# Performance work log

Measured on AMD Instinct MI355X. Metric: run time of the kernel, lower is better.

Reference implementation:

```python
import jax, jax.numpy as jnp
import numpy as np

HIDDEN = 1024
D_COMPLEX = HIDDEN // 2


def setup_inputs() -> dict:
    key = jax.random.key(0)
    ks = jax.random.split(key, 9)
    B, S, H = 4, 4096, HIDDEN
    scale = 1.0 / np.sqrt(H)
    inp = {
        "x": jax.random.normal(ks[0], (B, S, H), dtype=jnp.float32),
        "Wq": jax.random.normal(ks[1], (H, H), dtype=jnp.float32) * scale,
        "bq": jnp.zeros((H,), dtype=jnp.float32),
        "Wk": jax.random.normal(ks[2], (H, H), dtype=jnp.float32) * scale,
        "bk": jnp.zeros((H,), dtype=jnp.float32),
        "Wv": jax.random.normal(ks[3], (H, H), dtype=jnp.float32) * scale,
        "bv": jnp.zeros((H,), dtype=jnp.float32),
        "Wo": jax.random.normal(ks[4], (H, H), dtype=jnp.float32) * scale,
        "bo": jnp.zeros((H,), dtype=jnp.float32),
    }
    return inp


def reference(x, Wq, bq, Wk, bk, Wv, bv, Wo, bo):
    # torch.nn.Linear: y = x @ W.T + b
    Q = x @ Wq.T + bq  # [B,S,H]
    K = x @ Wk.T + bk
    V = x @ Wv.T + bv
    # Re(Q_c * conj(K_c)) summed over d_complex == Q_r.K_r + Q_i.K_i
    # == full real dot product over hidden dim.
    scores = jnp.einsum('bqd,bkd->bqk', Q, K) / np.sqrt(D_COMPLEX)
    weights = jax.nn.softmax(scores, axis=-1)  # [B,S,S]
    # to_real(weights @ V_c) = concat(weights@V_r, weights@V_i) = weights @ V
    out = jnp.einsum('bqk,bkd->bqd', weights, V)  # [B,S,H]
    return out @ Wo.T + bo
```

## Files before the change

kernel.cpp:

```cpp
#include <hip/hip_runtime.h>
#include <cstdint>
#include <cstddef>


typedef unsigned short ushort_t;
typedef __bf16 bf16x8 __attribute__((ext_vector_type(8)));
typedef float f32x4 __attribute__((ext_vector_type(4)));
typedef unsigned short ushort4v __attribute__((ext_vector_type(4)));

struct Ptr4 { const float* p[4]; };
struct BPtr4 { const ushort_t* p[4]; };
struct CPtr4 { void* p[4]; };
struct Bias4 { const float* p[4]; };
struct RS4 { float* p[4]; };
struct Alpha4 { float a[4]; };

__device__ __forceinline__ ushort_t f32_to_bf16(float f) {
  union { float f; unsigned int u; } x;
  x.f = f;
  unsigned int r = x.u + 0x7FFFu + ((x.u >> 16) & 1u);
  return (ushort_t)(r >> 16);
}

template <typename T> __device__ __forceinline__ T cvt_out(float v);
template <> __device__ __forceinline__ float cvt_out<float>(float v) { return v; }
template <> __device__ __forceinline__ ushort_t cvt_out<ushort_t>(float v) { return f32_to_bf16(v); }

__device__ __forceinline__ void gl2lds16(const ushort_t* g, ushort_t* l) {
  __builtin_amdgcn_global_load_lds(
      (__attribute__((address_space(1))) void*)(g),
      (__attribute__((address_space(3))) void*)(l),
      16, 0, 0);
}

__global__ __launch_bounds__(256) void cvt_f32_bf16(
    Ptr4 srcs, ushort_t* __restrict__ out0, size_t zstride, int n4) {
  int i = blockIdx.x * 256 + threadIdx.x;
  if (i >= n4) return;
  const float* in = srcs.p[blockIdx.z & 3];
  ushort_t* out = out0 + zstride * blockIdx.z;
  float4 f = reinterpret_cast<const float4*>(in)[i];
  ushort4v o;
  o.x = f32_to_bf16(f.x);
  o.y = f32_to_bf16(f.y);
  o.z = f32_to_bf16(f.z);
  o.w = f32_to_bf16(f.w);
  reinterpret_cast<ushort4v*>(out)[i] = o;
}

template <typename OutT, int EPI>
__global__ __launch_bounds__(512, 2) void gemm256(
    BPtr4 a4, BPtr4 b4, Bias4 bz, Alpha4 al, CPtr4 c4, RS4 rs4,
    int Klen, int lda, int ldb, int ldc) {
  __shared__ __align__(16) ushort_t lds[8 * 8192];

  const int z = blockIdx.z & 3;
  const ushort_t* __restrict__ A = a4.p[z];
  const ushort_t* __restrict__ B = b4.p[z];
  const float* bias = bz.p[z];
  const float alpha = al.a[z];
  OutT* __restrict__ C = (OutT*)c4.p[z];
  float* __restrict__ rsum = rs4.p[z];

  const int flat = blockIdx.x + gridDim.x * blockIdx.y;
  const int bandH = gridDim.y >> 3;
  const int xcd = flat & 7;
  const int slot = flat >> 3;
  const int bxs = slot / bandH;
  const int bys = xcd * bandH + (slot - bxs * bandH);
  const int blockRow = bys * 256;
  const int blockCol = bxs * 256;

  const int tid = threadIdx.x;
  const int lane = tid & 63;
  const int w = tid >> 6;
  const int wqm = w >> 2;
  const int wqn = w & 3;
  const int lm = lane & 15;
  const int quad = lane >> 4;
  const int swz = (lm & 7) * 8;
  const int rowA = wqm * 64 + lm;
  const int rowB = wqn * 32 + lm;

  const int rowb = w * 8 + (lane >> 3);
  const int csw = ((lane & 7) ^ (lane >> 3)) * 8;
  const ushort_t* pA = A + (size_t)(blockRow + rowb) * lda + csw;
  const ushort_t* pB = B + (size_t)(blockCol + rowb) * ldb + csw;
  ushort_t* ldsw = lds + rowb * 64 + (lane & 7) * 8;

#define STAGE_HALF(ts, ab, hh)                                               \
  do {                                                                       \
    const int ld_ = (ab) ? ldb : lda;                                        \
    const ushort_t* g_ =                                                     \
        ((ab) ? pB : pA) + (size_t)(hh) * 128 * ld_ + (size_t)(ts) * 64;     \
    ushort_t* l_ = ldsw + (((((ts) & 1) << 2) | ((ab) << 1) | (hh)) * 8192); \
    gl2lds16(g_, l_);                                                        \
    gl2lds16(g_ + (size_t)64 * ld_, l_ + 4096);                              \
  } while (0)

  bf16x8 af[4][2], bf[2][2];
  f32x4 acc[2][2][4][2] = {};

#define READ_A(BUF, MQ)                                                      \
  do {                                                                       \
    _Pragma("unroll") for (int i = 0; i < 4; ++i)                            \
    _Pragma("unroll") for (int kk = 0; kk < 2; ++kk)                         \
      af[i][kk] = *reinterpret_cast<const bf16x8*>(                          \
          &lds[((BUF) * 4 + (MQ)) * 8192 + (rowA + i * 16) * 64 +            \
               ((kk * 32 + quad * 8) ^ swz)]);                               \
  } while (0)

#define READ_B(BUF, NQ)                                                      \
  do {                                                                       \
    _Pragma("unroll") for (int j = 0; j < 2; ++j)                            \
    _Pragma("unroll") for (int kk = 0; kk < 2; ++kk)                         \
      bf[j][kk] = *reinterpret_cast<const bf16x8*>(                          \
          &lds[((BUF) * 4 + 2 + (NQ)) * 8192 + (rowB + j * 16) * 64 +        \
               ((kk * 32 + quad * 8) ^ swz)]);                               \
  } while (0)

#define MFMA_Q(MQ, NQ)                                                       \
  do {                                                                       \
    __builtin_amdgcn_s_setprio(1);                                           \
    _Pragma("unroll") for (int kk = 0; kk < 2; ++kk)                         \
    _Pragma("unroll") for (int i = 0; i < 4; ++i)                            \
    _Pragma("unroll") for (int j = 0; j < 2; ++j)                            \
      acc[MQ][NQ][i][j] = __builtin_amdgcn_mfma_f32_16x16x32_bf16(           \
          af[i][kk], bf[j][kk], acc[MQ][NQ][i][j], 0, 0, 0);                 \
    __builtin_amdgcn_s_setprio(0);                                           \
  } while (0)

#define BAR() __builtin_amdgcn_s_barrier()
#define VMW4() asm volatile("s_waitcnt vmcnt(4)" ::: "memory")
#define VMW0() asm volatile("s_waitcnt vmcnt(0)" ::: "memory")

  const int NT = Klen >> 6;

  STAGE_HALF(0, 0, 0); STAGE_HALF(0, 0, 1); STAGE_HALF(0, 1, 0); STAGE_HALF(0, 1, 1);
  STAGE_HALF(1, 0, 0); STAGE_HALF(1, 1, 1);
  VMW4();
  BAR();

  int t = 0;
  for (; t + 3 < NT; t += 2) {
    READ_A(0, 0); READ_B(0, 0); STAGE_HALF(t + 1, 0, 1); BAR(); MFMA_Q(0, 0); BAR();
    READ_B(0, 1);               STAGE_HALF(t + 1, 1, 0); BAR(); MFMA_Q(0, 1); BAR();
    READ_A(0, 1);               STAGE_HALF(t + 2, 0, 0); BAR(); MFMA_Q(1, 1); BAR();
    READ_B(0, 0);               STAGE_HALF(t + 2, 1, 1); BAR(); MFMA_Q(1, 0); VMW4(); BAR();
    READ_A(1, 0); READ_B(1, 0); STAGE_HALF(t + 2, 0, 1); BAR(); MFMA_Q(0, 0); BAR();
    READ_B(1, 1);               STAGE_HALF(t + 2, 1, 0); BAR(); MFMA_Q(0, 1); BAR();
    READ_A(1, 1);               STAGE_HALF(t + 3, 0, 0); BAR(); MFMA_Q(1, 1); BAR();
    READ_B(1, 0);               STAGE_HALF(t + 3, 1, 1); BAR(); MFMA_Q(1, 0); VMW4(); BAR();
  }

  READ_A(0, 0); READ_B(0, 0); STAGE_HALF(t + 1, 0, 1); BAR(); MFMA_Q(0, 0); BAR();
  READ_B(0, 1);               STAGE_HALF(t + 1, 1, 0); BAR(); MFMA_Q(0, 1); BAR();
  READ_A(0, 1);               BAR(); MFMA_Q(1, 1); BAR();
  READ_B(0, 0);               BAR(); MFMA_Q(1, 0); VMW0(); BAR();
  READ_A(1, 0); READ_B(1, 0); BAR(); MFMA_Q(0, 0); BAR();
  READ_B(1, 1);               BAR(); MFMA_Q(0, 1); BAR();
  READ_A(1, 1);               BAR(); MFMA_Q(1, 1); BAR();
  READ_B(1, 0);               BAR(); MFMA_Q(1, 0);

  if constexpr (EPI == 0) {
#pragma unroll
    for (int mq = 0; mq < 2; ++mq) {
#pragma unroll
      for (int nq = 0; nq < 2; ++nq) {
        const int mB = blockRow + mq * 128 + wqm * 64 + quad * 4;
        const int nB = blockCol + nq * 128 + wqn * 32 + lm;
#pragma unroll
        for (int j = 0; j < 2; ++j) {
          const int n = nB + j * 16;
          const float bv = bias ? bias[n] : 0.0f;
#pragma unroll
          for (int i = 0; i < 4; ++i) {
#pragma unroll
            for (int r = 0; r < 4; ++r) {
              const int m = mB + i * 16 + r;
              C[(size_t)m * ldc + n] =
                  cvt_out<OutT>(acc[mq][nq][i][j][r] * alpha + bv);
            }
          }
        }
      }
    }
  } else if constexpr (EPI == 1) {
#pragma unroll
    for (int mq = 0; mq < 2; ++mq) {
#pragma unroll
      for (int i = 0; i < 4; ++i) {
#pragma unroll
        for (int r = 0; r < 4; ++r) {
          const int m = blockRow + mq * 128 + wqm * 64 + quad * 4 + i * 16 + r;
          float psum = 0.0f;
#pragma unroll
          for (int nq = 0; nq < 2; ++nq) {
#pragma unroll
            for (int j = 0; j < 2; ++j) {
              const int n = blockCol + nq * 128 + wqn * 32 + lm + j * 16;
              const float e = __expf(acc[mq][nq][i][j][r] * alpha);
              psum += e;
              C[(size_t)m * ldc + n] = cvt_out<OutT>(e);
            }
          }
#pragma unroll
          for (int o = 8; o > 0; o >>= 1) psum += __shfl_xor(psum, o, 16);
          if (lm == 0) atomicAdd(&rsum[m], psum);
        }
      }
    }
  } else {
#pragma unroll
    for (int mq = 0; mq < 2; ++mq) {
#pragma unroll
      for (int i = 0; i < 4; ++i) {
#pragma unroll
        for (int r = 0; r < 4; ++r) {
          const int m = blockRow + mq * 128 + wqm * 64 + quad * 4 + i * 16 + r;
          const float inv = 1.0f / rsum[m];
#pragma unroll
          for (int nq = 0; nq < 2; ++nq) {
#pragma unroll
            for (int j = 0; j < 2; ++j) {
              const int n = blockCol + nq * 128 + wqn * 32 + lm + j * 16;
              C[(size_t)m * ldc + n] =
                  cvt_out<OutT>(acc[mq][nq][i][j][r] * inv);
            }
          }
        }
      }
    }
  }
#undef STAGE_HALF
#undef READ_A
#undef READ_B
#undef MFMA_Q
#undef BAR
#undef VMW4
#undef VMW0
}

__global__ __launch_bounds__(256) void transpose_bf16(
    const ushort_t* __restrict__ in, ushort_t* __restrict__ out, int rows,
    int cols) {
  __shared__ ushort_t tile[32][33];
  const size_t slab = (size_t)rows * cols;
  in += (size_t)blockIdx.z * slab;
  out += (size_t)blockIdx.z * slab;
  const int c0 = blockIdx.x * 32;
  const int r0 = blockIdx.y * 32;
  const int tx = threadIdx.x & 31;
  const int ty = threadIdx.x >> 5;
#pragma unroll
  for (int i = ty; i < 32; i += 8)
    tile[i][tx] = in[(size_t)(r0 + i) * cols + (c0 + tx)];
  __syncthreads();
#pragma unroll
  for (int i = ty; i < 32; i += 8)
    out[(size_t)(c0 + i) * rows + (r0 + tx)] = tile[tx][i];
}

extern "C" void kernel_launch(void* const* d_in, const int* in_sizes, int n_in,
                              void* d_out, int out_size, void* d_ws,
                              size_t ws_size, hipStream_t stream) {
  (void)in_sizes; (void)n_in; (void)out_size; (void)ws_size;

  const float* x  = (const float*)d_in[0];
  const float* Wq = (const float*)d_in[1];
  const float* bq = (const float*)d_in[2];
  const float* Wk = (const float*)d_in[3];
  const float* bk = (const float*)d_in[4];
  const float* Wv = (const float*)d_in[5];
  const float* bv = (const float*)d_in[6];
  const float* Wo = (const float*)d_in[7];
  const float* bo = (const float*)d_in[8];
  float* out = (float*)d_out;

  constexpr int BATCH = 4, S = 4096, H = 1024;
  constexpr int M = BATCH * S;
  constexpr size_t SZ_X = (size_t)M * H;
  constexpr size_t SZ_W = (size_t)H * H;
  constexpr size_t SH = (size_t)S * H;
  constexpr size_t SS = (size_t)S * S;
  constexpr float SCALE = 0.04419417382415922f;

  uint8_t* w = (uint8_t*)d_ws;
  ushort_t* xb  = (ushort_t*)w; w += SZ_X * 2;
  ushort_t* wqb = (ushort_t*)w; w += SZ_W * 2;
  ushort_t* wkb = (ushort_t*)w; w += SZ_W * 2;
  ushort_t* wvb = (ushort_t*)w; w += SZ_W * 2;
  ushort_t* wob = (ushort_t*)w; w += SZ_W * 2;
  ushort_t* Qb  = (ushort_t*)w; w += SZ_X * 2;
  ushort_t* Kb  = (ushort_t*)w; w += SZ_X * 2;
  ushort_t* Vb  = (ushort_t*)w; w += SZ_X * 2;
  ushort_t* VTb = (ushort_t*)w; w += SZ_X * 2;
  float* rsb = (float*)w; w += (size_t)M * 4;
  ushort_t* E0 = (ushort_t*)out;
  ushort_t* E1 = (ushort_t*)out + SS;
  ushort_t* E2 = xb;
  ushort_t* E3 = Vb;

  const dim3 blk(256);
  const dim3 blkG(512);
  const Bias4 nobias = {{nullptr, nullptr, nullptr, nullptr}};
  const Alpha4 ones = {{1.0f, 1.0f, 1.0f, 1.0f}};
  const RS4 nors = {{nullptr, nullptr, nullptr, nullptr}};

  {
    Ptr4 px = {{x, nullptr, nullptr, nullptr}};
    cvt_f32_bf16<<<dim3((unsigned)(SZ_X / 4 / 256), 1, 1), blk, 0, stream>>>(
        px, xb, 0, (int)(SZ_X / 4));
    Ptr4 pw = {{Wq, Wk, Wv, Wo}};
    cvt_f32_bf16<<<dim3((unsigned)(SZ_W / 4 / 256), 1, 4), blk, 0, stream>>>(
        pw, wqb, SZ_W, (int)(SZ_W / 4));
  }

  {
    BPtr4 a4 = {{xb, xb, xb, xb}};
    BPtr4 b4 = {{wqb, wkb, wvb, wqb}};
    Bias4 bqkv = {{bq, bk, bv, nullptr}};
    Alpha4 al = {{SCALE, 1.0f, 1.0f, 1.0f}};
    CPtr4 c4 = {{Qb, Kb, Vb, Qb}};
    gemm256<ushort_t, 0><<<dim3(H / 256, M / 256, 3), blkG, 0, stream>>>(
        a4, b4, bqkv, al, c4, nors, H, H, H, H);
  }

  transpose_bf16<<<dim3(H / 32, S / 32, BATCH), blk, 0, stream>>>(Vb, VTb, S, H);

  (void)hipMemsetAsync(rsb, 0, (size_t)M * 4, stream);
  {
    BPtr4 a4 = {{Qb, Qb + SH, Qb + 2 * SH, Qb + 3 * SH}};
    BPtr4 b4 = {{Kb, Kb + SH, Kb + 2 * SH, Kb + 3 * SH}};
    CPtr4 c4 = {{E0, E1, E2, E3}};
    RS4 rs = {{rsb, rsb + S, rsb + 2 * S, rsb + 3 * S}};
    gemm256<ushort_t, 1><<<dim3(S / 256, S / 256, 4), blkG, 0, stream>>>(
        a4, b4, nobias, ones, c4, rs, H, H, H, S);
  }

  {
    BPtr4 a4 = {{E0, E1, E2, E3}};
    BPtr4 b4 = {{VTb, VTb + SH, VTb + 2 * SH, VTb + 3 * SH}};
    CPtr4 c4 = {{Kb, Kb + SH, Kb + 2 * SH, Kb + 3 * SH}};
    RS4 rs = {{rsb, rsb + S, rsb + 2 * S, rsb + 3 * S}};
    gemm256<ushort_t, 2><<<dim3(H / 256, S / 256, 4), blkG, 0, stream>>>(
        a4, b4, nobias, ones, c4, rs, S, S, S, H);
  }

  {
    BPtr4 a4 = {{Kb, Kb, Kb, Kb}};
    BPtr4 b4 = {{wob, wob, wob, wob}};
    Bias4 bb = {{bo, nullptr, nullptr, nullptr}};
    CPtr4 c4 = {{out, out, out, out}};
    gemm256<float, 0><<<dim3(H / 256, M / 256, 1), blkG, 0, stream>>>(
        a4, b4, bb, ones, c4, nors, H, H, H, H);
  }
}
```

Measured before the change: 541.0 us.

## Pack bf16 epilogue stores, fold log2e into Q scale, permute columns

The bf16 GEMM epilogues now convert pairs of accumulators with v_cvt_pk_bf16_f32 and write one 32-bit word per lane instead of two scalar 16-bit stores. Storing lanes j=0 and j=1 side by side changes the column order of every output, so the V transpose and the Wo conversion apply a matching pi32 permutation to the reduction dimension to keep the final result correct. Folding log2(e) into the Q scale lets the softmax exponent use the hardware v_exp_f32 (exp2) directly. The cost is a strided, unvectorized write path in the Wo conversion, and the bias handling in the permuted Q/K/V layout has to stay consistent with the new column order.

New measurement: 554.8 us. +2.6%, slower.

```diff
diff --git a/kernel.cpp b/kernel.cpp
--- a/kernel.cpp
+++ b/kernel.cpp
@@ -22,6 +22,20 @@
   return (ushort_t)(r >> 16);
 }
 
+__device__ __forceinline__ unsigned int cvt_pk_bf16(float a, float b) {
+  unsigned int d;
+  asm("v_cvt_pk_bf16_f32 %0, %1, %2" : "=v"(d) : "v"(a), "v"(b));
+  return d;
+}
+
+__device__ __forceinline__ float exp2_hw(float x) {
+  float d;
+  asm("v_exp_f32 %0, %1" : "=v"(d) : "v"(x));
+  return d;
+}
+
+__device__ __forceinline__ int pi32(int c) { return 2 * (c & 15) + (c >> 4); }
+
 template <typename T> __device__ __forceinline__ T cvt_out(float v);
 template <> __device__ __forceinline__ float cvt_out<float>(float v) { return v; }
 template <> __device__ __forceinline__ ushort_t cvt_out<ushort_t>(float v) { return f32_to_bf16(v); }
@@ -34,18 +48,29 @@
 }
 
 __global__ __launch_bounds__(256) void cvt_f32_bf16(
-    Ptr4 srcs, ushort_t* __restrict__ out0, size_t zstride, int n4) {
+    Ptr4 srcs, ushort_t* __restrict__ out0, size_t zstride, int n4,
+    int permz) {
   int i = blockIdx.x * 256 + threadIdx.x;
   if (i >= n4) return;
   const float* in = srcs.p[blockIdx.z & 3];
   ushort_t* out = out0 + zstride * blockIdx.z;
   float4 f = reinterpret_cast<const float4*>(in)[i];
-  ushort4v o;
-  o.x = f32_to_bf16(f.x);
-  o.y = f32_to_bf16(f.y);
-  o.z = f32_to_bf16(f.z);
-  o.w = f32_to_bf16(f.w);
-  reinterpret_cast<ushort4v*>(out)[i] = o;
+  if ((int)blockIdx.z == permz) {
+    const float v[4] = {f.x, f.y, f.z, f.w};
+#pragma unroll
+    for (int e = 0; e < 4; ++e) {
+      int ff = i * 4 + e;
+      int c = ff & 31;
+      out[(ff & ~31) + pi32(pi32(c))] = f32_to_bf16(v[e]);
+    }
+  } else {
+    ushort4v o;
+    o.x = f32_to_bf16(f.x);
+    o.y = f32_to_bf16(f.y);
+    o.z = f32_to_bf16(f.z);
+    o.w = f32_to_bf16(f.w);
+    reinterpret_cast<ushort4v*>(out)[i] = o;
+  }
 }
 
 template <typename OutT, int EPI>
@@ -162,7 +187,29 @@
   READ_A(1, 1);               BAR(); MFMA_Q(1, 1); BAR();
   READ_B(1, 0);               BAR(); MFMA_Q(1, 0);
 
-  if constexpr (EPI == 0) {
+  constexpr bool kPack = (sizeof(OutT) == 2);
+  if constexpr (EPI == 0 && kPack) {
+#pragma unroll
+    for (int mq = 0; mq < 2; ++mq) {
+#pragma unroll
+      for (int nq = 0; nq < 2; ++nq) {
+        const int colBase = blockCol + nq * 128 + wqn * 32;
+        const float bv0 = bias ? bias[colBase + lm] : 0.0f;
+        const float bv1 = bias ? bias[colBase + lm + 16] : 0.0f;
+#pragma unroll
+        for (int i = 0; i < 4; ++i) {
+#pragma unroll
+          for (int r = 0; r < 4; ++r) {
+            const int m = blockRow + mq * 128 + wqm * 64 + quad * 4 + i * 16 + r;
+            const unsigned int pk =
+                cvt_pk_bf16(acc[mq][nq][i][0][r] * alpha + bv0,
+                            acc[mq][nq][i][1][r] * alpha + bv1);
+            reinterpret_cast<unsigned int*>(C + (size_t)m * ldc + colBase)[lm] = pk;
+          }
+        }
+      }
+    }
+  } else if constexpr (EPI == 0) {
 #pragma unroll
     for (int mq = 0; mq < 2; ++mq) {
 #pragma unroll
@@ -196,13 +243,12 @@
           float psum = 0.0f;
 #pragma unroll
           for (int nq = 0; nq < 2; ++nq) {
-#pragma unroll
-            for (int j = 0; j < 2; ++j) {
-              const int n = blockCol + nq * 128 + wqn * 32 + lm + j * 16;
-              const float e = __expf(acc[mq][nq][i][j][r] * alpha);
-              psum += e;
-              C[(size_t)m * ldc + n] = cvt_out<OutT>(e);
-            }
+            const int colBase = blockCol + nq * 128 + wqn * 32;
+            const float e0 = exp2_hw(acc[mq][nq][i][0][r]);
+            const float e1 = exp2_hw(acc[mq][nq][i][1][r]);
+            psum += e0 + e1;
+            reinterpret_cast<unsigned int*>(C + (size_t)m * ldc + colBase)[lm] =
+                cvt_pk_bf16(e0, e1);
           }
 #pragma unroll
           for (int o = 8; o > 0; o >>= 1) psum += __shfl_xor(psum, o, 16);
@@ -221,12 +267,10 @@
           const float inv = 1.0f / rsum[m];
 #pragma unroll
           for (int nq = 0; nq < 2; ++nq) {
-#pragma unroll
-            for (int j = 0; j < 2; ++j) {
-              const int n = blockCol + nq * 128 + wqn * 32 + lm + j * 16;
-              C[(size_t)m * ldc + n] =
-                  cvt_out<OutT>(acc[mq][nq][i][j][r] * inv);
-            }
+            const int colBase = blockCol + nq * 128 + wqn * 32;
+            reinterpret_cast<unsigned int*>(C + (size_t)m * ldc + colBase)[lm] =
+                cvt_pk_bf16(acc[mq][nq][i][0][r] * inv,
+                            acc[mq][nq][i][1][r] * inv);
           }
         }
       }
@@ -256,9 +300,10 @@
   for (int i = ty; i < 32; i += 8)
     tile[i][tx] = in[(size_t)(r0 + i) * cols + (c0 + tx)];
   __syncthreads();
+  const int txp = pi32(tx);
 #pragma unroll
   for (int i = ty; i < 32; i += 8)
-    out[(size_t)(c0 + i) * rows + (r0 + tx)] = tile[tx][i];
+    out[(size_t)(c0 + i) * rows + (r0 + txp)] = tile[tx][i];
 }
 
 extern "C" void kernel_launch(void* const* d_in, const int* in_sizes, int n_in,
@@ -283,7 +328,7 @@
   constexpr size_t SZ_W = (size_t)H * H;
   constexpr size_t SH = (size_t)S * H;
   constexpr size_t SS = (size_t)S * S;
-  constexpr float SCALE = 0.04419417382415922f;
+  constexpr float SCALE_L2E = 0.04419417382415922f * 1.4426950408889634f;
 
   uint8_t* w = (uint8_t*)d_ws;
   ushort_t* xb  = (ushort_t*)w; w += SZ_X * 2;
@@ -310,17 +355,17 @@
   {
     Ptr4 px = {{x, nullptr, nullptr, nullptr}};
     cvt_f32_bf16<<<dim3((unsigned)(SZ_X / 4 / 256), 1, 1), blk, 0, stream>>>(
-        px, xb, 0, (int)(SZ_X / 4));
+        px, xb, 0, (int)(SZ_X / 4), -1);
     Ptr4 pw = {{Wq, Wk, Wv, Wo}};
     cvt_f32_bf16<<<dim3((unsigned)(SZ_W / 4 / 256), 1, 4), blk, 0, stream>>>(
-        pw, wqb, SZ_W, (int)(SZ_W / 4));
+        pw, wqb, SZ_W, (int)(SZ_W / 4), 3);
   }
 
   {
     BPtr4 a4 = {{xb, xb, xb, xb}};
     BPtr4 b4 = {{wqb, wkb, wvb, wqb}};
     Bias4 bqkv = {{bq, bk, bv, nullptr}};
-    Alpha4 al = {{SCALE, 1.0f, 1.0f, 1.0f}};
+    Alpha4 al = {{SCALE_L2E, 1.0f, 1.0f, 1.0f}};
     CPtr4 c4 = {{Qb, Kb, Vb, Qb}};
     gemm256<ushort_t, 0><<<dim3(H / 256, M / 256, 3), blkG, 0, stream>>>(
         a4, b4, bqkv, al, c4, nors, H, H, H, H);
```
